# Kernel optimization log

Hardware: AMD Instinct MI355X
Metric: run time of the kernel (lower is better)

Reference implementation:

```python
import jax, jax.numpy as jnp
import numpy as np

DIM, NUM_HEADS, N_POINTS = 256, 8, 4
N_Q, N_KV = 32768, 32768


def setup_inputs() -> dict:
    key = jax.random.key(0)
    ks = jax.random.split(key, 16)
    C, H, P = DIM, NUM_HEADS, N_POINTS
    s = 1.0 / np.sqrt(C)
    inp = {
        "query": jax.random.normal(ks[0], (N_Q, C), jnp.float32),
        "key": jax.random.normal(ks[1], (N_KV, C), jnp.float32),
        "value": jax.random.normal(ks[2], (N_KV, C), jnp.float32),
        # reference_points: Linear(C, 2*H*P)
        "Wr": jax.random.normal(ks[3], (C, 2 * H * P), jnp.float32) * s,
        "br": jnp.zeros((2 * H * P,), jnp.float32),
        # offset_attn: Linear(C, H*P*2)
        "Wo": jax.random.normal(ks[4], (C, H * P * 2), jnp.float32) * s,
        "bo": jnp.zeros((H * P * 2,), jnp.float32),
        # value_proj: Linear(C, C)
        "Wv": jax.random.normal(ks[5], (C, C), jnp.float32) * s,
        "bv": jnp.zeros((C,), jnp.float32),
        # output_proj: Linear(C, C)
        "Wout": jax.random.normal(ks[6], (C, C), jnp.float32) * s,
        "bout": jnp.zeros((C,), jnp.float32),
    }
    return inp


def reference(query, key, value, Wr, br, Wo, bo, Wv, bv, Wout, bout):
    N, C = query.shape
    M = value.shape[0]
    H, P = NUM_HEADS, N_POINTS
    Ch = C // H

    # sampling locations in [0,1] (ref) plus unconstrained offsets
    ref = jax.nn.sigmoid((query @ Wr + br).reshape(N, H, P, 2))
    off = (query @ Wo + bo).reshape(N, H, P, 2)
    loc = ref + off                              # [N,H,P,2]

    # 1-D bilinear interpolation along the token axis. The original's
    # 4-term (wx,wy) expression algebraically collapses to a pure lerp in x:
    # (1-wx)(1-wy)+ (1-wx)wy = (1-wx), wx(1-wy)+wx*wy = wx.
    x = loc[..., 0] * (M - 1)                    # [N,H,P]
    x0 = jnp.clip(jnp.floor(x).astype(jnp.int32), 0, M - 1)
    x1 = jnp.clip(x0 + 1, 0, M - 1)
    wx = (x - x0.astype(x.dtype))[..., None]     # [N,H,P,1]

    hidx = jnp.arange(H)[None, :, None]          # head-aligned gather index

    def sample(table):                           # table: [M,H,Ch]
        g0 = table[x0, hidx]                     # [N,H,P,Ch]
        g1 = table[x1, hidx]
        return (1.0 - wx) * g0 + wx * g1

    v = (value @ Wv + bv).reshape(M, H, Ch)      # value_proj, split heads
    sv = sample(v)                               # [N,H,P,Ch] sampled values

    # attention weights from query/key: sample per-head keys at the same
    # locations, dot with per-head queries, softmax over the P points
    k = key.reshape(M, H, Ch)
    sk = sample(k)                               # [N,H,P,Ch]
    q = query.reshape(N, H, Ch)
    scores = jnp.einsum("nhc,nhpc->nhp", q, sk) / jnp.sqrt(
        jnp.asarray(Ch, query.dtype)
    )
    attn = jax.nn.softmax(scores, axis=-1)       # [N,H,P]

    out = jnp.einsum("nhp,nhpc->nhc", attn, sv).reshape(N, C)
    return out @ Wout + bout
```

## Files before the change

### kernel.cpp

```cpp
#include <hip/hip_runtime.h>
#include <hip/hip_bf16.h>
#include <stdint.h>

#define NQ    32768
#define NKV   32768
#define CDIM  256
#define NHEADS 8
#define NPTS  4

using bf16x8 = __attribute__((ext_vector_type(8))) short;
using f32x4  = __attribute__((ext_vector_type(4))) float;
using u16x8  = __attribute__((ext_vector_type(8))) ushort;

static __device__ __forceinline__ ushort f2bf(float f) {
  uint32_t u = __float_as_uint(f);
  return (ushort)((u + 0x7FFFu + ((u >> 16) & 1u)) >> 16);
}
static __device__ __forceinline__ float bf2f(ushort h) {
  return __uint_as_float(((uint32_t)h) << 16);
}
static __device__ __forceinline__ void async16(const void* g, void* l) {
  __builtin_amdgcn_global_load_lds(
      (const __attribute__((address_space(1))) uint32_t*)g,
      (__attribute__((address_space(3))) uint32_t*)l, 16, 0, 0);
}
static __device__ __forceinline__ void async16_sc0(const void* g, void* l) {
  __builtin_amdgcn_global_load_lds(
      (const __attribute__((address_space(1))) uint32_t*)g,
      (__attribute__((address_space(3))) uint32_t*)l, 16, 0, 1);
}
#define WAIT_VM(N) do { asm volatile("s_waitcnt vmcnt(" #N ")" ::: "memory"); \
                        __builtin_amdgcn_sched_barrier(0); } while (0)

__global__ __launch_bounds__(256) void transpose_w(const float* __restrict__ W,
                                                   ushort* __restrict__ WT) {
  int j = blockIdx.x, k = threadIdx.x;
  WT[j * 256 + k] = f2bf(W[k * 256 + j]);
}

__global__ __launch_bounds__(256) void gemm_mfma(
    const ushort* __restrict__ A, const ushort* __restrict__ BT,
    const float* __restrict__ bias, ushort* __restrict__ Cb,
    float* __restrict__ Cf, int out_bf16) {
  __shared__ ushort Alds[128 * 32];
  __shared__ ushort Blds[128 * 32];
  const int t = threadIdx.x;
  const int wave = t >> 6, lane = t & 63;
  const int mt = blockIdx.x >> 1, nt = blockIdx.x & 1;
  const int m0 = mt * 128, n0 = nt * 128;
  const int wr = wave >> 1, wc = wave & 1;
  const int r16 = lane & 15, kb = (lane >> 4) * 8;

  f32x4 acc[4][4] = {};

  for (int kt = 0; kt < 256; kt += 32) {
    __syncthreads();
#pragma unroll
    for (int it = 0; it < 2; ++it) {
      int c = it * 256 + t;
      int row = c >> 2, cc = c & 3;
      async16(A  + ((size_t)(m0 + row) * 256 + kt + cc * 8),
              Alds + (size_t)(it * 256 + wave * 64) * 8);
      async16(BT + ((size_t)(n0 + row) * 256 + kt + cc * 8),
              Blds + (size_t)(it * 256 + wave * 64) * 8);
    }
    __syncthreads();

    bf16x8 af[4], bfr[4];
#pragma unroll
    for (int m = 0; m < 4; ++m)
      af[m] = *(const bf16x8*)&Alds[(wr * 64 + m * 16 + r16) * 32 + kb];
#pragma unroll
    for (int n = 0; n < 4; ++n)
      bfr[n] = *(const bf16x8*)&Blds[(wc * 64 + n * 16 + r16) * 32 + kb];
#pragma unroll
    for (int m = 0; m < 4; ++m)
#pragma unroll
      for (int n = 0; n < 4; ++n)
        acc[m][n] = __builtin_amdgcn_mfma_f32_16x16x32_bf16(af[m], bfr[n],
                                                            acc[m][n], 0, 0, 0);
  }

  const int rg = lane >> 4;
#pragma unroll
  for (int m = 0; m < 4; ++m)
#pragma unroll
    for (int n = 0; n < 4; ++n) {
      int gc = n0 + wc * 64 + n * 16 + r16;
      float bb = bias[gc];
#pragma unroll
      for (int r = 0; r < 4; ++r) {
        int gr = m0 + wr * 64 + m * 16 + rg * 4 + r;
        float v = acc[m][n][r] + bb;
        if (out_bf16) Cb[(size_t)gr * 256 + gc] = f2bf(v);
        else          Cf[(size_t)gr * 256 + gc] = v;
      }
    }
}

__global__ __launch_bounds__(256) void gemm_mfma_fa(
    const float* __restrict__ Af, const ushort* __restrict__ BT,
    const float* __restrict__ bias, ushort* __restrict__ CbT) {
  __shared__ ushort S[128 * 64];
  ushort* Alds = S;
  ushort* Blds = S + 128 * 32;
  const int t = threadIdx.x;
  const int wave = t >> 6, lane = t & 63;
  const int mt = blockIdx.x >> 1, nt = blockIdx.x & 1;
  const int m0 = mt * 128, n0 = nt * 128;
  const int wr = wave >> 1, wc = wave & 1;
  const int r16 = lane & 15, kb = (lane >> 4) * 8;

  f32x4 acc[4][4] = {};

  for (int kt = 0; kt < 256; kt += 32) {
    __syncthreads();
#pragma unroll
    for (int it = 0; it < 2; ++it) {
      int c = it * 256 + t;
      int row = c >> 2, cc = c & 3;
      async16(BT + ((size_t)(n0 + row) * 256 + kt + cc * 8),
              Blds + (size_t)(it * 256 + wave * 64) * 8);
    }
#pragma unroll
    for (int it = 0; it < 2; ++it) {
      int c = it * 256 + t;
      int row = c >> 2, cc = c & 3;
      const float* src = Af + (size_t)(m0 + row) * 256 + kt + cc * 8;
      f32x4 a = *(const f32x4*)src;
      f32x4 b = *(const f32x4*)(src + 4);
      u16x8 w;
#pragma unroll
      for (int e = 0; e < 4; ++e) { w[e] = f2bf(a[e]); w[4 + e] = f2bf(b[e]); }
      *(u16x8*)&Alds[(size_t)c * 8] = w;
    }
    __syncthreads();

    bf16x8 af[4], bfr[4];
#pragma unroll
    for (int m = 0; m < 4; ++m)
      af[m] = *(const bf16x8*)&Alds[(wr * 64 + m * 16 + r16) * 32 + kb];
#pragma unroll
    for (int n = 0; n < 4; ++n)
      bfr[n] = *(const bf16x8*)&Blds[(wc * 64 + n * 16 + r16) * 32 + kb];
#pragma unroll
    for (int m = 0; m < 4; ++m)
#pragma unroll
      for (int n = 0; n < 4; ++n)
        acc[m][n] = __builtin_amdgcn_mfma_f32_16x16x32_bf16(af[m], bfr[n],
                                                            acc[m][n], 0, 0, 0);
  }

  const int rg = lane >> 4;
  const int h0 = n0 >> 5;
#pragma unroll
  for (int pass = 0; pass < 2; ++pass) {
    __syncthreads();
    if (wc == pass) {
#pragma unroll
      for (int m = 0; m < 4; ++m)
#pragma unroll
        for (int nn = 0; nn < 4; ++nn) {
          int col = nn * 16 + r16;
          int hh = col >> 5, ch = col & 31;
          float bb = bias[n0 + wc * 64 + col];
#pragma unroll
          for (int r = 0; r < 4; ++r) {
            int row = wr * 64 + m * 16 + rg * 4 + r;
            S[(hh * 128 + row) * 32 + ch] = f2bf(acc[m][nn][r] + bb);
          }
        }
    }
    __syncthreads();
#pragma unroll
    for (int i = 0; i < 4; ++i) {
      int chunk = i * 256 + t;
      int hh = chunk >> 9;
      int within = chunk & 511;
      u16x8 w = *(const u16x8*)&S[chunk * 8];
      ushort* dst = CbT + ((size_t)(h0 + pass * 2 + hh) * NKV + m0) * 32;
      *(u16x8*)(dst + within * 8) = w;
    }
  }
}

__global__ __launch_bounds__(256) void loc_gemm(const float* __restrict__ Q,
                                                const float* __restrict__ Wr,
                                                const float* __restrict__ Wo,
                                                float* __restrict__ locr) {
  __shared__ float AT[64][68];
  __shared__ float Bl[64][64];
  const int m0 = blockIdx.x * 64;
  const int t = threadIdx.x;
  const int tr = t >> 4, tc = t & 15;
  float acc[4][4] = {};

  for (int k0 = 0; k0 < 256; k0 += 64) {
    __syncthreads();
#pragma unroll
    for (int i = 0; i < 4; ++i) {
      int row = (t >> 4) + 16 * i;
      int kk = (t & 15) * 4;
      float4 v = *(const float4*)&Q[(size_t)(m0 + row) * 256 + k0 + kk];
      AT[kk + 0][row] = v.x; AT[kk + 1][row] = v.y;
      AT[kk + 2][row] = v.z; AT[kk + 3][row] = v.w;
    }
#pragma unroll
    for (int i = 0; i < 16; ++i) {
      int j = t & 63;
      int kk = (t >> 6) + 4 * i;
      float v = (j < 32) ? Wr[(size_t)(k0 + kk) * 64 + 2 * j]
                         : Wo[(size_t)(k0 + kk) * 64 + 2 * (j - 32)];
      Bl[kk][j] = v;
    }
    __syncthreads();
#pragma unroll 8
    for (int kk = 0; kk < 64; ++kk) {
      float4 a = *(const float4*)&AT[kk][tr * 4];
      float4 b = *(const float4*)&Bl[kk][tc * 4];
      float av[4] = {a.x, a.y, a.z, a.w};
      float bv4[4] = {b.x, b.y, b.z, b.w};
#pragma unroll
      for (int i = 0; i < 4; ++i)
#pragma unroll
        for (int jj = 0; jj < 4; ++jj) acc[i][jj] += av[i] * bv4[jj];
    }
  }
#pragma unroll
  for (int i = 0; i < 4; ++i)
#pragma unroll
    for (int jj = 0; jj < 4; ++jj)
      locr[(size_t)(m0 + tr * 4 + i) * 64 + tc * 4 + jj] = acc[i][jj];
}

__global__ __launch_bounds__(256, 4) void sample_attn(
    const float* __restrict__ query, const float* __restrict__ key,
    const ushort* __restrict__ vtabT, const float* __restrict__ locr,
    const float* __restrict__ br, const float* __restrict__ bo,
    ushort* __restrict__ out2) {
  __shared__ char smem[4][4096];
  const int wave = threadIdx.x >> 6, l = threadIdx.x & 63;
  const int j = l & 31;
  const int n = blockIdx.x * 4 + wave;
  const int Mm1 = NKV - 1;
  char* vbuf = smem[wave];

  float rr = locr[(size_t)n * 64 + j];
  float oo = locr[(size_t)n * 64 + 32 + j];
  float ref = 1.0f / (1.0f + expf(-(rr + br[2 * j])));
  float x = (ref + (oo + bo[2 * j])) * (float)Mm1;
  float xf = floorf(x);
  int x0 = (int)fminf(fmaxf(xf, 0.0f), (float)Mm1);
  int x1 = (x0 + 1 > Mm1) ? Mm1 : x0 + 1;
  float wx = x - (float)x0;
  float w0 = 1.0f - wx;

  {
    const int pg3 = l >> 3, c7 = l & 7;
    const int sc = c7 ^ pg3;
#pragma unroll
    for (int i = 0; i < 4; ++i) {
      int pg = i * 8 + pg3;
      int row = __shfl(x0, pg, 64);
      async16_sc0(vtabT + ((size_t)(pg >> 2) * NKV + row) * 32 + sc * 8,
                  vbuf + i * 1024);
    }
  }
  __builtin_amdgcn_sched_barrier(0);

  const int myrow = (l < 32) ? x0 : x1;
  const float* kr = key + (size_t)myrow * 256 + (j >> 2) * 32;
  f32x4 kv0, kv1, kv2, kv3, kv4, kv5, kv6, kv7;
  asm volatile("global_load_dwordx4 %0, %1, off sc0"            : "=v"(kv0) : "v"(kr) : "memory");
  asm volatile("global_load_dwordx4 %0, %1, off offset:16 sc0"  : "=v"(kv1) : "v"(kr) : "memory");
  asm volatile("global_load_dwordx4 %0, %1, off offset:32 sc0"  : "=v"(kv2) : "v"(kr) : "memory");
  asm volatile("global_load_dwordx4 %0, %1, off offset:48 sc0"  : "=v"(kv3) : "v"(kr) : "memory");
  asm volatile("global_load_dwordx4 %0, %1, off offset:64 sc0"  : "=v"(kv4) : "v"(kr) : "memory");
  asm volatile("global_load_dwordx4 %0, %1, off offset:80 sc0"  : "=v"(kv5) : "v"(kr) : "memory");
  asm volatile("global_load_dwordx4 %0, %1, off offset:96 sc0"  : "=v"(kv6) : "v"(kr) : "memory");
  asm volatile("global_load_dwordx4 %0, %1, off offset:112 sc0" : "=v"(kv7) : "v"(kr) : "memory");

  const float* qr = query + (size_t)n * 256 + (j >> 2) * 32;
  f32x4 qv[8];
#pragma unroll
  for (int c = 0; c < 8; ++c) qv[c] = *(const f32x4*)(qr + c * 4);

  WAIT_VM(0);

  float dot = 0.f;
#pragma unroll
  for (int e = 0; e < 4; ++e) {
    dot += qv[0][e] * kv0[e]; dot += qv[1][e] * kv1[e];
    dot += qv[2][e] * kv2[e]; dot += qv[3][e] * kv3[e];
    dot += qv[4][e] * kv4[e]; dot += qv[5][e] * kv5[e];
    dot += qv[6][e] * kv6[e]; dot += qv[7][e] * kv7[e];
  }

  float other = __shfl_xor(dot, 32, 64);
  float d0 = (l < 32) ? dot : other;
  float d1 = (l < 32) ? other : dot;
  float score = (w0 * d0 + wx * d1) * 0.17677669529663687f;

  float m1 = fmaxf(score, __shfl_xor(score, 1, 64));
  float mx = fmaxf(m1, __shfl_xor(m1, 2, 64));
  float e0 = expf(score - mx);
  float s1 = e0 + __shfl_xor(e0, 1, 64);
  float ssum = s1 + __shfl_xor(s1, 2, 64);
  float attn = e0 / ssum;
  int edge = (x0 == Mm1);
  float c1v = edge ? 0.0f : attn * wx;
  float c0v = edge ? attn * (w0 + wx) : attn * w0;

  const int oh = l >> 3, os = l & 7;
  float cc0[4], cc1[4];
#pragma unroll
  for (int m = 0; m < 4; ++m) {
    cc0[m] = __shfl(c0v, oh * 4 + m, 64);
    cc1[m] = __shfl(c1v, oh * 4 + m, 64);
  }

  float acc[4] = {};
#pragma unroll
  for (int m = 0; m < 4; ++m) {
    int pt = oh * 4 + m;
    int pos0 = (os >> 1) ^ (pt & 7);
    int pos1 = (4 + (os >> 1)) ^ (pt & 7);
    const char* pb = vbuf + pt * 128 + (os & 1) * 8;
    ushort4 v0 = *(const ushort4*)(pb + pos0 * 16);
    ushort4 v1 = *(const ushort4*)(pb + pos1 * 16);
#pragma unroll
    for (int e = 0; e < 4; ++e)
      acc[e] += cc0[m] * bf2f((&v0.x)[e]) + cc1[m] * bf2f((&v1.x)[e]);
  }
  ushort4 ow;
#pragma unroll
  for (int e = 0; e < 4; ++e) (&ow.x)[e] = f2bf(acc[e]);
  *(ushort4*)(out2 + (size_t)n * 256 + oh * 32 + os * 4) = ow;
}

extern "C" void kernel_launch(void* const* d_in, const int* in_sizes, int n_in,
                              void* d_out, int out_size, void* d_ws, size_t ws_size,
                              hipStream_t stream) {
  const float* query = (const float*)d_in[0];
  const float* key   = (const float*)d_in[1];
  const float* value = (const float*)d_in[2];
  const float* Wr    = (const float*)d_in[3];
  const float* br    = (const float*)d_in[4];
  const float* Wo    = (const float*)d_in[5];
  const float* bo    = (const float*)d_in[6];
  const float* Wv    = (const float*)d_in[7];
  const float* bv    = (const float*)d_in[8];
  const float* Wout  = (const float*)d_in[9];
  const float* bout  = (const float*)d_in[10];
  float* out = (float*)d_out;

  char* ws = (char*)d_ws;
  ushort* out2  = (ushort*)(ws);
  ushort* vtabT = (ushort*)(ws + (16u << 20));
  float*  locr  = (float*) (ws + (32u << 20));
  ushort* WvT   = (ushort*)(ws + (40u << 20));
  ushort* WoT   = (ushort*)(ws + (40u << 20) + (1u << 17));

  transpose_w<<<256, 256, 0, stream>>>(Wv, WvT);
  transpose_w<<<256, 256, 0, stream>>>(Wout, WoT);
  gemm_mfma_fa<<<(NQ / 128) * 2, 256, 0, stream>>>(value, WvT, bv, vtabT);
  loc_gemm<<<NQ / 64, 256, 0, stream>>>(query, Wr, Wo, locr);
  sample_attn<<<NQ / 4, 256, 0, stream>>>(query, key, vtabT, locr, br, bo, out2);
  gemm_mfma<<<(NQ / 128) * 2, 256, 0, stream>>>(out2, WoT, bout, nullptr, out, 0);
}
```

Before: 103.0 us.

## Merge kernels and overlap output GEMM with second half of sampling

Merges the two weight transposes into one launch and co-schedules the value-projection GEMM with the location GEMM in a single kernel. The sampling-attention pass is split into two query halves so the output-projection GEMM for the first half runs in the same launch as attention for the second half. The attention body also drops the sc0 cache hints and the inline-asm loads, and moves the wait on the async value gather to after the softmax so the gather overlaps the score computation. This trades fewer launches and better overlap for a branchy heterogeneous kernel that shares one LDS allocation and loses the previous launch-bounds occupancy hint.

```diff
diff --git a/kernel.cpp b/kernel.cpp
--- a/kernel.cpp
+++ b/kernel.cpp
@@ -7,6 +7,7 @@
 #define CDIM  256
 #define NHEADS 8
 #define NPTS  4
+#define NHALF (NQ / 2)
 
 using bf16x8 = __attribute__((ext_vector_type(8))) short;
 using f32x4  = __attribute__((ext_vector_type(4))) float;
@@ -24,30 +25,27 @@
       (const __attribute__((address_space(1))) uint32_t*)g,
       (__attribute__((address_space(3))) uint32_t*)l, 16, 0, 0);
 }
-static __device__ __forceinline__ void async16_sc0(const void* g, void* l) {
-  __builtin_amdgcn_global_load_lds(
-      (const __attribute__((address_space(1))) uint32_t*)g,
-      (__attribute__((address_space(3))) uint32_t*)l, 16, 0, 1);
-}
 #define WAIT_VM(N) do { asm volatile("s_waitcnt vmcnt(" #N ")" ::: "memory"); \
                         __builtin_amdgcn_sched_barrier(0); } while (0)
 
-__global__ __launch_bounds__(256) void transpose_w(const float* __restrict__ W,
-                                                   ushort* __restrict__ WT) {
-  int j = blockIdx.x, k = threadIdx.x;
-  WT[j * 256 + k] = f2bf(W[k * 256 + j]);
-}
-
-__global__ __launch_bounds__(256) void gemm_mfma(
+__global__ __launch_bounds__(256) void transpose_both(
+    const float* __restrict__ Wv, const float* __restrict__ Wout,
+    ushort* __restrict__ WvT, ushort* __restrict__ WoT) {
+  int b = blockIdx.x, k = threadIdx.x;
+  if (b < 256) WvT[b * 256 + k] = f2bf(Wv[k * 256 + b]);
+  else { int j = b - 256; WoT[j * 256 + k] = f2bf(Wout[k * 256 + j]); }
+}
+
+static __device__ __forceinline__ void gemm_body(
     const ushort* __restrict__ A, const ushort* __restrict__ BT,
-    const float* __restrict__ bias, ushort* __restrict__ Cb,
-    float* __restrict__ Cf, int out_bf16) {
-  __shared__ ushort Alds[128 * 32];
-  __shared__ ushort Blds[128 * 32];
+    const float* __restrict__ bias, float* __restrict__ Cf,
+    char* smem, int bid, int moff) {
+  ushort* Alds = (ushort*)smem;
+  ushort* Blds = (ushort*)smem + 128 * 32;
   const int t = threadIdx.x;
   const int wave = t >> 6, lane = t & 63;
-  const int mt = blockIdx.x >> 1, nt = blockIdx.x & 1;
-  const int m0 = mt * 128, n0 = nt * 128;
+  const int mt = bid >> 1, nt = bid & 1;
+  const int m0 = moff + mt * 128, n0 = nt * 128;
   const int wr = wave >> 1, wc = wave & 1;
   const int r16 = lane & 15, kb = (lane >> 4) * 8;
 
@@ -61,7 +59,7 @@
       int row = c >> 2, cc = c & 3;
       async16(A  + ((size_t)(m0 + row) * 256 + kt + cc * 8),
               Alds + (size_t)(it * 256 + wave * 64) * 8);
-      async16(BT + ((size_t)(n0 + row) * 256 + kt + cc * 8),
+      async16(BT + ((size_t)((nt * 128) + row) * 256 + kt + cc * 8),
               Blds + (size_t)(it * 256 + wave * 64) * 8);
     }
     __syncthreads();
@@ -91,22 +89,21 @@
 #pragma unroll
       for (int r = 0; r < 4; ++r) {
         int gr = m0 + wr * 64 + m * 16 + rg * 4 + r;
-        float v = acc[m][n][r] + bb;
-        if (out_bf16) Cb[(size_t)gr * 256 + gc] = f2bf(v);
-        else          Cf[(size_t)gr * 256 + gc] = v;
+        Cf[(size_t)gr * 256 + gc] = acc[m][n][r] + bb;
       }
     }
 }
 
-__global__ __launch_bounds__(256) void gemm_mfma_fa(
+static __device__ __forceinline__ void fa_body(
     const float* __restrict__ Af, const ushort* __restrict__ BT,
-    const float* __restrict__ bias, ushort* __restrict__ CbT) {
-  __shared__ ushort S[128 * 64];
+    const float* __restrict__ bias, ushort* __restrict__ CbT,
+    char* smem, int bid) {
+  ushort* S = (ushort*)smem;
   ushort* Alds = S;
   ushort* Blds = S + 128 * 32;
   const int t = threadIdx.x;
   const int wave = t >> 6, lane = t & 63;
-  const int mt = blockIdx.x >> 1, nt = blockIdx.x & 1;
+  const int mt = bid >> 1, nt = bid & 1;
   const int m0 = mt * 128, n0 = nt * 128;
   const int wr = wave >> 1, wc = wave & 1;
   const int r16 = lane & 15, kb = (lane >> 4) * 8;
@@ -184,13 +181,13 @@
   }
 }
 
-__global__ __launch_bounds__(256) void loc_gemm(const float* __restrict__ Q,
-                                                const float* __restrict__ Wr,
-                                                const float* __restrict__ Wo,
-                                                float* __restrict__ locr) {
-  __shared__ float AT[64][68];
-  __shared__ float Bl[64][64];
-  const int m0 = blockIdx.x * 64;
+static __device__ __forceinline__ void loc_body(
+    const float* __restrict__ Q, const float* __restrict__ Wr,
+    const float* __restrict__ Wo, float* __restrict__ locr,
+    char* smem, int bid) {
+  float (*AT)[68] = (float(*)[68])smem;
+  float (*Bl)[64] = (float(*)[64])(smem + 64 * 68 * 4);
+  const int m0 = bid * 64;
   const int t = threadIdx.x;
   const int tr = t >> 4, tc = t & 15;
   float acc[4][4] = {};
@@ -233,17 +230,16 @@
       locr[(size_t)(m0 + tr * 4 + i) * 64 + tc * 4 + jj] = acc[i][jj];
 }
 
-__global__ __launch_bounds__(256, 4) void sample_attn(
+static __device__ __forceinline__ void attn_body(
     const float* __restrict__ query, const float* __restrict__ key,
     const ushort* __restrict__ vtabT, const float* __restrict__ locr,
     const float* __restrict__ br, const float* __restrict__ bo,
-    ushort* __restrict__ out2) {
-  __shared__ char smem[4][4096];
+    ushort* __restrict__ out2, char* smem, int bid, int n0q) {
   const int wave = threadIdx.x >> 6, l = threadIdx.x & 63;
   const int j = l & 31;
-  const int n = blockIdx.x * 4 + wave;
+  const int n = n0q + bid * 4 + wave;
   const int Mm1 = NKV - 1;
-  char* vbuf = smem[wave];
+  char* vbuf = smem + wave * 4096;
 
   float rr = locr[(size_t)n * 64 + j];
   float oo = locr[(size_t)n * 64 + 32 + j];
@@ -262,39 +258,27 @@
     for (int i = 0; i < 4; ++i) {
       int pg = i * 8 + pg3;
       int row = __shfl(x0, pg, 64);
-      async16_sc0(vtabT + ((size_t)(pg >> 2) * NKV + row) * 32 + sc * 8,
-                  vbuf + i * 1024);
+      async16(vtabT + ((size_t)(pg >> 2) * NKV + row) * 32 + sc * 8,
+              vbuf + i * 1024);
     }
   }
   __builtin_amdgcn_sched_barrier(0);
 
   const int myrow = (l < 32) ? x0 : x1;
   const float* kr = key + (size_t)myrow * 256 + (j >> 2) * 32;
-  f32x4 kv0, kv1, kv2, kv3, kv4, kv5, kv6, kv7;
-  asm volatile("global_load_dwordx4 %0, %1, off sc0"            : "=v"(kv0) : "v"(kr) : "memory");
-  asm volatile("global_load_dwordx4 %0, %1, off offset:16 sc0"  : "=v"(kv1) : "v"(kr) : "memory");
-  asm volatile("global_load_dwordx4 %0, %1, off offset:32 sc0"  : "=v"(kv2) : "v"(kr) : "memory");
-  asm volatile("global_load_dwordx4 %0, %1, off offset:48 sc0"  : "=v"(kv3) : "v"(kr) : "memory");
-  asm volatile("global_load_dwordx4 %0, %1, off offset:64 sc0"  : "=v"(kv4) : "v"(kr) : "memory");
-  asm volatile("global_load_dwordx4 %0, %1, off offset:80 sc0"  : "=v"(kv5) : "v"(kr) : "memory");
-  asm volatile("global_load_dwordx4 %0, %1, off offset:96 sc0"  : "=v"(kv6) : "v"(kr) : "memory");
-  asm volatile("global_load_dwordx4 %0, %1, off offset:112 sc0" : "=v"(kv7) : "v"(kr) : "memory");
-
   const float* qr = query + (size_t)n * 256 + (j >> 2) * 32;
-  f32x4 qv[8];
+  f32x4 kv[8], qv[8];
+#pragma unroll
+  for (int c = 0; c < 8; ++c) kv[c] = *(const f32x4*)(kr + c * 4);
 #pragma unroll
   for (int c = 0; c < 8; ++c) qv[c] = *(const f32x4*)(qr + c * 4);
-
-  WAIT_VM(0);
+  __builtin_amdgcn_sched_barrier(0);
 
   float dot = 0.f;
 #pragma unroll
-  for (int e = 0; e < 4; ++e) {
-    dot += qv[0][e] * kv0[e]; dot += qv[1][e] * kv1[e];
-    dot += qv[2][e] * kv2[e]; dot += qv[3][e] * kv3[e];
-    dot += qv[4][e] * kv4[e]; dot += qv[5][e] * kv5[e];
-    dot += qv[6][e] * kv6[e]; dot += qv[7][e] * kv7[e];
-  }
+  for (int c = 0; c < 8; ++c)
+#pragma unroll
+    for (int e = 0; e < 4; ++e) dot += qv[c][e] * kv[c][e];
 
   float other = __shfl_xor(dot, 32, 64);
   float d0 = (l < 32) ? dot : other;
@@ -319,6 +303,8 @@
     cc1[m] = __shfl(c1v, oh * 4 + m, 64);
   }
 
+  WAIT_VM(0);
+
   float acc[4] = {};
 #pragma unroll
   for (int m = 0; m < 4; ++m) {
@@ -336,6 +322,46 @@
 #pragma unroll
   for (int e = 0; e < 4; ++e) (&ow.x)[e] = f2bf(acc[e]);
   *(ushort4*)(out2 + (size_t)n * 256 + oh * 32 + os * 4) = ow;
+}
+
+__global__ __launch_bounds__(256) void k_fa_loc(
+    const float* __restrict__ value, const ushort* __restrict__ WvT,
+    const float* __restrict__ bv, ushort* __restrict__ vtabT,
+    const float* __restrict__ query, const float* __restrict__ Wr,
+    const float* __restrict__ Wo, float* __restrict__ locr) {
+  __shared__ __align__(16) char smem[34048];
+  int b = blockIdx.x;
+  if (b < 512) fa_body(value, WvT, bv, vtabT, smem, b);
+  else         loc_body(query, Wr, Wo, locr, smem, b - 512);
+}
+
+__global__ __launch_bounds__(256) void k_attn0(
+    const float* __restrict__ query, const float* __restrict__ key,
+    const ushort* __restrict__ vtabT, const float* __restrict__ locr,
+    const float* __restrict__ br, const float* __restrict__ bo,
+    ushort* __restrict__ out2) {
+  __shared__ __align__(16) char smem[16384];
+  attn_body(query, key, vtabT, locr, br, bo, out2, smem, blockIdx.x, 0);
+}
+
+__global__ __launch_bounds__(256) void k_mid(
+    const ushort* __restrict__ out2, const ushort* __restrict__ WoT,
+    const float* __restrict__ bout, float* __restrict__ out,
+    const float* __restrict__ query, const float* __restrict__ key,
+    const ushort* __restrict__ vtabT, const float* __restrict__ locr,
+    const float* __restrict__ br, const float* __restrict__ bo,
+    ushort* __restrict__ out2w) {
+  __shared__ __align__(16) char smem[16384];
+  int b = blockIdx.x;
+  if (b < 256) gemm_body(out2, WoT, bout, out, smem, b, 0);
+  else attn_body(query, key, vtabT, locr, br, bo, out2w, smem, b - 256, NHALF);
+}
+
+__global__ __launch_bounds__(256) void k_out1(
+    const ushort* __restrict__ out2, const ushort* __restrict__ WoT,
+    const float* __restrict__ bout, float* __restrict__ out) {
+  __shared__ __align__(16) char smem[16384];
+  gemm_body(out2, WoT, bout, out, smem, blockIdx.x, NHALF);
 }
 
 extern "C" void kernel_launch(void* const* d_in, const int* in_sizes, int n_in,
@@ -361,10 +387,12 @@
   ushort* WvT   = (ushort*)(ws + (40u << 20));
   ushort* WoT   = (ushort*)(ws + (40u << 20) + (1u << 17));
 
-  transpose_w<<<256, 256, 0, stream>>>(Wv, WvT);
-  transpose_w<<<256, 256, 0, stream>>>(Wout, WoT);
-  gemm_mfma_fa<<<(NQ / 128) * 2, 256, 0, stream>>>(value, WvT, bv, vtabT);
-  loc_gemm<<<NQ / 64, 256, 0, stream>>>(query, Wr, Wo, locr);
-  sample_attn<<<NQ / 4, 256, 0, stream>>>(query, key, vtabT, locr, br, bo, out2);
-  gemm_mfma<<<(NQ / 128) * 2, 256, 0, stream>>>(out2, WoT, bout, nullptr, out, 0);
-}
+  transpose_both<<<512, 256, 0, stream>>>(Wv, Wout, WvT, WoT);
+  k_fa_loc<<<1024, 256, 0, stream>>>(value, WvT, bv, vtabT,
+                                     query, Wr, Wo, locr);
+  k_attn0<<<NHALF / 4, 256, 0, stream>>>(query, key, vtabT, locr, br, bo, out2);
+  k_mid<<<256 + NHALF / 4, 256, 0, stream>>>(out2, WoT, bout, out,
+                                             query, key, vtabT, locr, br, bo,
+                                             out2);
+  k_out1<<<256, 256, 0, stream>>>(out2, WoT, bout, out);
+}
```

Result: slower. 109.3 us (+6.1%).
